# Optimization experiments

Measured on AMD Instinct MI355X. Metric: run time of the kernel, lower is better.

## Reference

```python
import jax, jax.numpy as jnp
import numpy as np

D_K = 64  # per-head dim, used as softmax scale (matches __init__ d_k)

def setup_inputs() -> dict:
    key = jax.random.key(0)
    kq, kk, kv, km = jax.random.split(key, 4)
    B, H, S, D = 2, 16, 2048, D_K
    q = jax.random.normal(kq, (B, H, S, D), dtype=jnp.float32)
    k = jax.random.normal(kk, (B, H, S, D), dtype=jnp.float32)
    v = jax.random.normal(kv, (B, H, S, D), dtype=jnp.float32)
    mask = jax.random.randint(km, (B, 1, S, S), 0, 2).astype(jnp.bool_)
    return {"q": q, "k": k, "v": v, "mask": mask}

def reference(q, k, v, mask):
    # attn = (q / sqrt(d_k)) @ k^T  -> [B,H,S,S]
    scale = 1.0 / jnp.sqrt(jnp.float32(D_K))
    attn = jnp.einsum("bhqd,bhkd->bhqk", q * scale, k)
    # faithful to torch masked_fill(mask, -1e-09) -- note tiny value, not -1e9
    attn = jnp.where(mask, jnp.float32(-1e-9), attn)
    weights = jax.nn.softmax(attn, axis=-1)  # dropout p=0.0 -> identity
    output = jnp.einsum("bhqk,bhkd->bhqd", weights, v)
    return (output, weights)
```

## Files before the change

### kernel.cpp

```cpp
#include <hip/hip_runtime.h>
#include <hip/hip_bf16.h>


namespace {

constexpr int kS = 2048;
constexpr int kD = 64;
constexpr int kBH = 32;
constexpr int kTQW = 16;
constexpr int kNW = 4;
constexpr int kTQB = kTQW * kNW;
constexpr int kChunk = 64;
constexpr int kNB = kBH * (kS / kTQB);
constexpr size_t kWOff = (size_t)kBH * kS * kD;

typedef __attribute__((ext_vector_type(8))) short bf16x8;
typedef __attribute__((ext_vector_type(4))) float f32x4;

__device__ inline short f2bf(float f) {
  union { float f; unsigned u; } x; x.f = f;
  return (short)((x.u + 0x7fffu + ((x.u >> 16) & 1u)) >> 16);
}

__device__ inline bf16x8 load8_bf16(const float* p, float scale) {
  float4 x0 = *(const float4*)p;
  float4 x1 = *(const float4*)(p + 4);
  bf16x8 f;
  f[0] = f2bf(x0.x * scale); f[1] = f2bf(x0.y * scale);
  f[2] = f2bf(x0.z * scale); f[3] = f2bf(x0.w * scale);
  f[4] = f2bf(x1.x * scale); f[5] = f2bf(x1.y * scale);
  f[6] = f2bf(x1.z * scale); f[7] = f2bf(x1.w * scale);
  return f;
}

__global__ __launch_bounds__(256, 4) void attn_fused(
    const float* __restrict__ qg, const float* __restrict__ kg,
    const float* __restrict__ vg, const unsigned int* __restrict__ mg,
    float* __restrict__ outg) {
  __shared__ __align__(16) short Kt[kChunk][72];
  __shared__ __align__(16) short Vt[kD][72];
  __shared__ __align__(16) short Wt[kNW][kTQW][72];
  __shared__ __align__(16) unsigned char Msk[kChunk][80];

  const int tid  = threadIdx.x;
  const int wv   = tid >> 6;
  const int lane = tid & 63;
  const int l15  = lane & 15;
  const int quad = lane >> 4;

  const int bid  = blockIdx.x;
  const int work = ((bid & 7) << 7) | (bid >> 3);
  const int qt   = work & 31;
  const int bh   = work >> 5;
  const int b    = bh >> 4;
  const int q0b  = qt * kTQB;

  int allW32 = 1, allI32 = 1, allBF = 1;
#pragma unroll
  for (int i = 0; i < 64; ++i) {
    const unsigned u = mg[i];
    const unsigned lo = u & 0xFFFFu, hi = u >> 16;
    allW32 &= (int)(u == 0u || u == 0x3F800000u);
    allI32 &= (int)(u == 0u || u == 1u);
    allBF  &= (int)((lo == 0u || lo == 0x3F80u) && (hi == 0u || hi == 0x3F80u));
  }
  int msz;
  if (allI32)      msz = 4;
  else if (allW32) msz = 4;
  else if (allBF)  msz = 2;
  else             msz = 1;
  const unsigned char* mB = (const unsigned char*)mg + (size_t)b * kS * kS * msz;

  const float* qbase = qg + (size_t)bh * kS * kD;
  const float* kbase = kg + (size_t)bh * kS * kD;
  const float* vbase = vg + (size_t)bh * kS * kD;
  float* obase = outg + (size_t)bh * kS * kD;
  float* wbase = outg + kWOff + (size_t)bh * kS * kS;

  bf16x8 aq[2];
#pragma unroll
  for (int dh = 0; dh < 2; ++dh)
    aq[dh] = load8_bf16(qbase + (size_t)(q0b + wv * kTQW + l15) * kD + dh * 32 + quad * 8, 0.125f);

  const int si = tid >> 2;
  const int sj = (tid & 3) << 4;

  auto stage_k = [&](int k0) {
    const float* p = kbase + (size_t)(k0 + si) * kD + sj;
    *(bf16x8*)&Kt[si][sj]     = load8_bf16(p, 1.0f);
    *(bf16x8*)&Kt[si][sj + 8] = load8_bf16(p + 8, 1.0f);
  };

  auto stage_v = [&](int k0) {
    const float* p = vbase + (size_t)(k0 + si) * kD + sj;
#pragma unroll
    for (int i = 0; i < 4; ++i) {
      float4 x = *(const float4*)(p + 4 * i);
      Vt[sj + 4 * i + 0][si] = f2bf(x.x);
      Vt[sj + 4 * i + 1][si] = f2bf(x.y);
      Vt[sj + 4 * i + 2][si] = f2bf(x.z);
      Vt[sj + 4 * i + 3][si] = f2bf(x.w);
    }
  };

  auto stage_mask = [&](int k0) {
    const size_t eoff = (size_t)(q0b + si) * kS + (size_t)(k0 + sj);
    if (msz == 1) {
      *(uint4*)&Msk[si][sj] = *(const uint4*)(mB + eoff);
    } else if (msz == 4) {
      const unsigned int* p = (const unsigned int*)mB + eoff;
      unsigned int* dst = (unsigned int*)&Msk[si][sj];
#pragma unroll
      for (int g = 0; g < 4; ++g) {
        uint4 e = *(const uint4*)(p + 4 * g);
        dst[g] = (e.x ? 1u : 0u) | ((e.y ? 1u : 0u) << 8) |
                 ((e.z ? 1u : 0u) << 16) | ((e.w ? 1u : 0u) << 24);
      }
    } else {
      const unsigned int* p = (const unsigned int*)((const unsigned short*)mB + eoff);
      unsigned int* dst = (unsigned int*)&Msk[si][sj];
#pragma unroll
      for (int g = 0; g < 4; ++g) {
        const unsigned int a = p[2 * g], c = p[2 * g + 1];
        dst[g] = ((a & 0xFFFFu) ? 1u : 0u) | (((a >> 16) ? 1u : 0u) << 8) |
                 (((c & 0xFFFFu) ? 1u : 0u) << 16) | (((c >> 16) ? 1u : 0u) << 24);
      }
    }
  };

  float lsum[4] = {0.f, 0.f, 0.f, 0.f};
  for (int k0 = 0; k0 < kS; k0 += kChunk) {
    __syncthreads();
    stage_k(k0);
    stage_mask(k0);
    __syncthreads();
#pragma unroll
    for (int cg = 0; cg < 4; ++cg) {
      bf16x8 bk0 = *(const bf16x8*)&Kt[cg * 16 + l15][quad * 8];
      bf16x8 bk1 = *(const bf16x8*)&Kt[cg * 16 + l15][32 + quad * 8];
      f32x4 acc = {0.f, 0.f, 0.f, 0.f};
      acc = __builtin_amdgcn_mfma_f32_16x16x32_bf16(aq[0], bk0, acc, 0, 0, 0);
      acc = __builtin_amdgcn_mfma_f32_16x16x32_bf16(aq[1], bk1, acc, 0, 0, 0);
#pragma unroll
      for (int r = 0; r < 4; ++r) {
        const int lrow = wv * kTQW + quad * 4 + r;
        const float e = __expf(acc[r]);
        lsum[r] += (Msk[lrow][cg * 16 + l15] != 0) ? 1.0f : e;
      }
    }
  }

  float inv_l[4];
#pragma unroll
  for (int r = 0; r < 4; ++r) {
    float t = lsum[r];
    t += __shfl_xor(t, 1, 16);
    t += __shfl_xor(t, 2, 16);
    t += __shfl_xor(t, 4, 16);
    t += __shfl_xor(t, 8, 16);
    inv_l[r] = 1.0f / t;
  }

  f32x4 acco[4];
#pragma unroll
  for (int d = 0; d < 4; ++d) acco[d] = (f32x4){0.f, 0.f, 0.f, 0.f};

  for (int k0 = 0; k0 < kS; k0 += kChunk) {
    __syncthreads();
    stage_k(k0);
    stage_v(k0);
    stage_mask(k0);
    __syncthreads();
#pragma unroll
    for (int cg = 0; cg < 4; ++cg) {
      bf16x8 bk0 = *(const bf16x8*)&Kt[cg * 16 + l15][quad * 8];
      bf16x8 bk1 = *(const bf16x8*)&Kt[cg * 16 + l15][32 + quad * 8];
      f32x4 acc = {0.f, 0.f, 0.f, 0.f};
      acc = __builtin_amdgcn_mfma_f32_16x16x32_bf16(aq[0], bk0, acc, 0, 0, 0);
      acc = __builtin_amdgcn_mfma_f32_16x16x32_bf16(aq[1], bk1, acc, 0, 0, 0);
      const int kcol = k0 + cg * 16 + l15;
#pragma unroll
      for (int r = 0; r < 4; ++r) {
        const int lrow = wv * kTQW + quad * 4 + r;
        const float e = __expf(acc[r]);
        const float w = ((Msk[lrow][cg * 16 + l15] != 0) ? 1.0f : e) * inv_l[r];
        wbase[(size_t)(q0b + lrow) * kS + kcol] = w;
        Wt[wv][quad * 4 + r][cg * 16 + l15] = f2bf(w);
      }
    }
#pragma unroll
    for (int ks = 0; ks < 2; ++ks) {
      bf16x8 aw = *(const bf16x8*)&Wt[wv][l15][ks * 32 + quad * 8];
#pragma unroll
      for (int d = 0; d < 4; ++d) {
        bf16x8 bv = *(const bf16x8*)&Vt[d * 16 + l15][ks * 32 + quad * 8];
        acco[d] = __builtin_amdgcn_mfma_f32_16x16x32_bf16(aw, bv, acco[d], 0, 0, 0);
      }
    }
  }

#pragma unroll
  for (int d = 0; d < 4; ++d)
#pragma unroll
    for (int r = 0; r < 4; ++r)
      obase[(size_t)(q0b + wv * kTQW + quad * 4 + r) * kD + d * 16 + l15] = acco[d][r];
}

}

extern "C" void kernel_launch(void* const* d_in, const int* in_sizes, int n_in,
                              void* d_out, int out_size, void* d_ws, size_t ws_size,
                              hipStream_t stream) {
  const float* q = (const float*)d_in[0];
  const float* k = (const float*)d_in[1];
  const float* v = (const float*)d_in[2];
  const unsigned int* mask = (const unsigned int*)d_in[3];
  float* out = (float*)d_out;
  attn_fused<<<dim3(kNB), dim3(256), 0, stream>>>(q, k, v, mask, out);
}
```

Baseline: 812.9 us.

## Register-prefetch next K/V/mask chunk, swizzle V transpose, nontemporal output stores

```diff
diff --git a/kernel.cpp b/kernel.cpp
--- a/kernel.cpp
+++ b/kernel.cpp
@@ -11,6 +11,7 @@
 constexpr int kNW = 4;
 constexpr int kTQB = kTQW * kNW;
 constexpr int kChunk = 64;
+constexpr int kNC = kS / kChunk;
 constexpr int kNB = kBH * (kS / kTQB);
 constexpr size_t kWOff = (size_t)kBH * kS * kD;
 
@@ -22,14 +23,12 @@
   return (short)((x.u + 0x7fffu + ((x.u >> 16) & 1u)) >> 16);
 }
 
-__device__ inline bf16x8 load8_bf16(const float* p, float scale) {
-  float4 x0 = *(const float4*)p;
-  float4 x1 = *(const float4*)(p + 4);
+__device__ inline bf16x8 cvt8(float4 a, float4 b, float scale) {
   bf16x8 f;
-  f[0] = f2bf(x0.x * scale); f[1] = f2bf(x0.y * scale);
-  f[2] = f2bf(x0.z * scale); f[3] = f2bf(x0.w * scale);
-  f[4] = f2bf(x1.x * scale); f[5] = f2bf(x1.y * scale);
-  f[6] = f2bf(x1.z * scale); f[7] = f2bf(x1.w * scale);
+  f[0] = f2bf(a.x * scale); f[1] = f2bf(a.y * scale);
+  f[2] = f2bf(a.z * scale); f[3] = f2bf(a.w * scale);
+  f[4] = f2bf(b.x * scale); f[5] = f2bf(b.y * scale);
+  f[6] = f2bf(b.z * scale); f[7] = f2bf(b.w * scale);
   return f;
 }
 
@@ -79,35 +78,60 @@
 
   bf16x8 aq[2];
 #pragma unroll
-  for (int dh = 0; dh < 2; ++dh)
-    aq[dh] = load8_bf16(qbase + (size_t)(q0b + wv * kTQW + l15) * kD + dh * 32 + quad * 8, 0.125f);
+  for (int dh = 0; dh < 2; ++dh) {
+    const float* p = qbase + (size_t)(q0b + wv * kTQW + l15) * kD + dh * 32 + quad * 8;
+    aq[dh] = cvt8(*(const float4*)p, *(const float4*)(p + 4), 0.125f);
+  }
 
   const int si = tid >> 2;
   const int sj = (tid & 3) << 4;
-
-  auto stage_k = [&](int k0) {
+  const int vd = (tid & 7) << 3;
+  const int vk = (tid >> 3) << 1;
+
+  float4 rk[4], rv[4];
+  uint4 rmq;
+
+  auto k_issue = [&](int k0) {
     const float* p = kbase + (size_t)(k0 + si) * kD + sj;
-    *(bf16x8*)&Kt[si][sj]     = load8_bf16(p, 1.0f);
-    *(bf16x8*)&Kt[si][sj + 8] = load8_bf16(p + 8, 1.0f);
-  };
-
-  auto stage_v = [&](int k0) {
-    const float* p = vbase + (size_t)(k0 + si) * kD + sj;
-#pragma unroll
-    for (int i = 0; i < 4; ++i) {
-      float4 x = *(const float4*)(p + 4 * i);
-      Vt[sj + 4 * i + 0][si] = f2bf(x.x);
-      Vt[sj + 4 * i + 1][si] = f2bf(x.y);
-      Vt[sj + 4 * i + 2][si] = f2bf(x.z);
-      Vt[sj + 4 * i + 3][si] = f2bf(x.w);
-    }
-  };
-
-  auto stage_mask = [&](int k0) {
-    const size_t eoff = (size_t)(q0b + si) * kS + (size_t)(k0 + sj);
+    rk[0] = ((const float4*)p)[0];
+    rk[1] = *(const float4*)(p + 4);
+    rk[2] = *(const float4*)(p + 8);
+    rk[3] = *(const float4*)(p + 12);
+  };
+  auto k_write = [&]() {
+    *(bf16x8*)&Kt[si][sj]     = cvt8(rk[0], rk[1], 1.0f);
+    *(bf16x8*)&Kt[si][sj + 8] = cvt8(rk[2], rk[3], 1.0f);
+  };
+
+  auto v_issue = [&](int k0) {
+    const float* p = vbase + (size_t)(k0 + vk) * kD + vd;
+    rv[0] = ((const float4*)p)[0];
+    rv[1] = *(const float4*)(p + 4);
+    rv[2] = *(const float4*)(p + kD);
+    rv[3] = *(const float4*)(p + kD + 4);
+  };
+  auto v_write = [&]() {
+    const float* lo = (const float*)&rv[0];
+    const float* hi = (const float*)&rv[2];
+#pragma unroll
+    for (int d = 0; d < 8; ++d) {
+      const int dd = vd + d;
+      const int ps = (vk >> 1) ^ (((dd >> 3) & 7) << 2);
+      const unsigned u = (unsigned)(unsigned short)f2bf(lo[d]) |
+                         ((unsigned)(unsigned short)f2bf(hi[d]) << 16);
+      *(unsigned*)&Vt[dd][2 * ps] = u;
+    }
+  };
+
+  auto m_issue = [&](int k0) {
+    if (msz == 1)
+      rmq = *(const uint4*)(mB + (size_t)(q0b + si) * kS + (size_t)(k0 + sj));
+  };
+  auto m_write = [&](int k0) {
     if (msz == 1) {
-      *(uint4*)&Msk[si][sj] = *(const uint4*)(mB + eoff);
+      *(uint4*)&Msk[si][sj] = rmq;
     } else if (msz == 4) {
+      const size_t eoff = (size_t)(q0b + si) * kS + (size_t)(k0 + sj);
       const unsigned int* p = (const unsigned int*)mB + eoff;
       unsigned int* dst = (unsigned int*)&Msk[si][sj];
 #pragma unroll
@@ -117,6 +141,7 @@
                  ((e.z ? 1u : 0u) << 16) | ((e.w ? 1u : 0u) << 24);
       }
     } else {
+      const size_t eoff = (size_t)(q0b + si) * kS + (size_t)(k0 + sj);
       const unsigned int* p = (const unsigned int*)((const unsigned short*)mB + eoff);
       unsigned int* dst = (unsigned int*)&Msk[si][sj];
 #pragma unroll
@@ -129,10 +154,14 @@
   };
 
   float lsum[4] = {0.f, 0.f, 0.f, 0.f};
-  for (int k0 = 0; k0 < kS; k0 += kChunk) {
-    __syncthreads();
-    stage_k(k0);
-    stage_mask(k0);
+  k_issue(0);
+  m_issue(0);
+  for (int c = 0; c < kNC; ++c) {
+    const int k0 = c * kChunk;
+    __syncthreads();
+    k_write();
+    m_write(k0);
+    if (c + 1 < kNC) { k_issue(k0 + kChunk); m_issue(k0 + kChunk); }
     __syncthreads();
 #pragma unroll
     for (int cg = 0; cg < 4; ++cg) {
@@ -149,6 +178,10 @@
       }
     }
   }
+
+  k_issue(0);
+  v_issue(0);
+  m_issue(0);
 
   float inv_l[4];
 #pragma unroll
@@ -165,11 +198,13 @@
 #pragma unroll
   for (int d = 0; d < 4; ++d) acco[d] = (f32x4){0.f, 0.f, 0.f, 0.f};
 
-  for (int k0 = 0; k0 < kS; k0 += kChunk) {
-    __syncthreads();
-    stage_k(k0);
-    stage_v(k0);
-    stage_mask(k0);
+  for (int c = 0; c < kNC; ++c) {
+    const int k0 = c * kChunk;
+    __syncthreads();
+    k_write();
+    v_write();
+    m_write(k0);
+    if (c + 1 < kNC) { k_issue(k0 + kChunk); v_issue(k0 + kChunk); m_issue(k0 + kChunk); }
     __syncthreads();
 #pragma unroll
     for (int cg = 0; cg < 4; ++cg) {
@@ -184,7 +219,7 @@
         const int lrow = wv * kTQW + quad * 4 + r;
         const float e = __expf(acc[r]);
         const float w = ((Msk[lrow][cg * 16 + l15] != 0) ? 1.0f : e) * inv_l[r];
-        wbase[(size_t)(q0b + lrow) * kS + kcol] = w;
+        __builtin_nontemporal_store(w, &wbase[(size_t)(q0b + lrow) * kS + kcol]);
         Wt[wv][quad * 4 + r][cg * 16 + l15] = f2bf(w);
       }
     }
@@ -193,7 +228,9 @@
       bf16x8 aw = *(const bf16x8*)&Wt[wv][l15][ks * 32 + quad * 8];
 #pragma unroll
       for (int d = 0; d < 4; ++d) {
-        bf16x8 bv = *(const bf16x8*)&Vt[d * 16 + l15][ks * 32 + quad * 8];
+        const int dd = d * 16 + l15;
+        const int psb = (ks * 16 + quad * 4) ^ (((dd >> 3) & 7) << 2);
+        bf16x8 bv = *(const bf16x8*)&Vt[dd][2 * psb];
         acco[d] = __builtin_amdgcn_mfma_f32_16x16x32_bf16(aw, bv, acco[d], 0, 0, 0);
       }
     }
@@ -203,7 +240,9 @@
   for (int d = 0; d < 4; ++d)
 #pragma unroll
     for (int r = 0; r < 4; ++r)
-      obase[(size_t)(q0b + wv * kTQW + quad * 4 + r) * kD + d * 16 + l15] = acco[d][r];
+      __builtin_nontemporal_store(
+          acco[d][r],
+          &obase[(size_t)(q0b + wv * kTQW + quad * 4 + r) * kD + d * 16 + l15]);
 }
 
 }
```

After: 790.9 us. -2.7%, faster.
